# Kernel tuning notes

Hardware: AMD Instinct MI355X
Metric: run time of the kernel (lower is better)

## Reference

```python
import jax, jax.numpy as jnp
import numpy as np

NEG = -1000000.0  # mask value used by the original module


def setup_inputs() -> dict:
    key = jax.random.key(0)
    ks = jax.random.split(key, 8)
    N, D_IN, D_Q, D_K, E = 8192, 512, 512, 512, 262144
    s = 1.0 / np.sqrt(D_IN)
    return {
        "x": jax.random.normal(ks[0], (N, D_IN), dtype=jnp.float32),
        "edge_index": jax.random.randint(ks[1], (2, E), 0, N, dtype=jnp.int64),
        "Wq": jax.random.normal(ks[2], (D_IN, D_Q), dtype=jnp.float32) * s,
        "bq": jax.random.normal(ks[3], (D_Q,), dtype=jnp.float32) * 0.01,
        "Wk": jax.random.normal(ks[4], (D_IN, D_K), dtype=jnp.float32) * s,
        "bk": jax.random.normal(ks[5], (D_K,), dtype=jnp.float32) * 0.01,
        "Wv": jax.random.normal(ks[6], (D_IN, D_K), dtype=jnp.float32) * s,
        "bv": jax.random.normal(ks[7], (D_K,), dtype=jnp.float32) * 0.01,
    }


def reference(x, edge_index, Wq, bq, Wk, bk, Wv, bv):
    # Linear projections (x: [N, D_in])
    q = x @ Wq + bq  # [N, Dq]
    k = x @ Wk + bk  # [N, Dk]
    v = x @ Wv + bv  # [N, Dk]

    N = x.shape[0]
    # Dense adjacency from edge list (matches torch scatter adjacency[e0, e1] = 1)
    adj = jnp.zeros((N, N), dtype=x.dtype).at[edge_index[0], edge_index[1]].set(1.0)

    # Full scores (ptr=None branch), scaled by sqrt(Dq)
    a = (q @ k.T) / jnp.sqrt(jnp.asarray(q.shape[-1], dtype=x.dtype))
    a = a * adj + (1.0 - adj) * NEG

    attn = jax.nn.softmax(a, axis=-1)  # [N, N]
    return attn @ v  # [N, Dk]
```

## Files before the change

kernel.cpp:

```cpp
#include <hip/hip_runtime.h>


#define N_NODES 8192
#define DIM 512
#define MASK_WORDS 256
#define SCAP 256

typedef __attribute__((ext_vector_type(8))) short short8;
typedef __attribute__((ext_vector_type(4))) float f32x4;

__device__ __forceinline__ unsigned short f2bf(float f) {
    unsigned int u = __float_as_uint(f);
    u += 0x7fffu + ((u >> 16) & 1u);
    return (unsigned short)(u >> 16);
}
__device__ __forceinline__ float bf_lo(unsigned int w) { return __uint_as_float(w << 16); }
__device__ __forceinline__ float bf_hi(unsigned int w) { return __uint_as_float(w & 0xffff0000u); }

__device__ __forceinline__ float wred_sum(float s) {
    #pragma unroll
    for (int off = 1; off <= 32; off <<= 1) s += __shfl_xor(s, off, 64);
    return s;
}
__device__ __forceinline__ float wred_max(float s) {
    #pragma unroll
    for (int off = 1; off <= 32; off <<= 1) s = fmaxf(s, __shfl_xor(s, off, 64));
    return s;
}
__device__ __forceinline__ int wred_sumi(int s) {
    #pragma unroll
    for (int off = 1; off <= 32; off <<= 1) s += __shfl_xor(s, off, 64);
    return s;
}
__device__ __forceinline__ float dot8(uint4 a, uint4 b) {
    return bf_lo(a.x) * bf_lo(b.x) + bf_hi(a.x) * bf_hi(b.x)
         + bf_lo(a.y) * bf_lo(b.y) + bf_hi(a.y) * bf_hi(b.y)
         + bf_lo(a.z) * bf_lo(b.z) + bf_hi(a.z) * bf_hi(b.z)
         + bf_lo(a.w) * bf_lo(b.w) + bf_hi(a.w) * bf_hi(b.w);
}

__global__ __launch_bounds__(256) void prep1(
    const float* __restrict__ x, unsigned short* __restrict__ xb,
    const float* __restrict__ Wq, const float* __restrict__ Wk,
    const float* __restrict__ Wv, unsigned short* __restrict__ Wt,
    unsigned int* __restrict__ mask)
{
    __shared__ float sm[32][33];
    const int b = blockIdx.x;
    if (b < 4096) {
        int i = b * 256 + threadIdx.x;
        float4 f = ((const float4*)x)[i];
        ushort4 o;
        o.x = f2bf(f.x); o.y = f2bf(f.y); o.z = f2bf(f.z); o.w = f2bf(f.w);
        ((ushort4*)xb)[i] = o;
        ((uint2*)mask)[i] = make_uint2(0u, 0u);
    } else {
        int bb = b - 4096;
        int which = bb >> 8, t = bb & 255;
        const float* __restrict__ W = (which == 0) ? Wq : (which == 1) ? Wk : Wv;
        unsigned short* __restrict__ outp = Wt + (size_t)which * DIM * DIM;
        int n0 = (t & 15) * 32, k0 = (t >> 4) * 32;
        int tx = threadIdx.x & 31, ty = threadIdx.x >> 5;
        #pragma unroll
        for (int r = 0; r < 4; ++r)
            sm[ty + 8 * r][tx] = W[(size_t)(k0 + ty + 8 * r) * DIM + n0 + tx];
        __syncthreads();
        #pragma unroll
        for (int r = 0; r < 4; ++r)
            outp[(size_t)(n0 + ty + 8 * r) * DIM + k0 + tx] = f2bf(sm[tx][ty + 8 * r]);
    }
}

__global__ __launch_bounds__(256) void prep2(
    const int* __restrict__ ei, unsigned int* __restrict__ mask, int E)
{
    int e = blockIdx.x * 256 + threadIdx.x;
    if (e >= E) return;
    int src = ei[e];
    int dst = ei[E + e];
    atomicOr(&mask[(size_t)src * MASK_WORDS + (dst >> 5)], 1u << (dst & 31));
}

__device__ __forceinline__ void load_lds16(const unsigned short* g, unsigned short* l) {
    __builtin_amdgcn_global_load_lds(
        (const __attribute__((address_space(1))) unsigned int*)g,
        (__attribute__((address_space(3))) unsigned int*)l, 16, 0, 0);
}

__global__ __launch_bounds__(256) void mfma_gemm(
    const unsigned short* __restrict__ xb, const unsigned short* __restrict__ Wt,
    const float* __restrict__ bq, const float* __restrict__ bk, const float* __restrict__ bv,
    unsigned short* __restrict__ qkv)
{
    const int p = blockIdx.x;
    const int xcd = p & 7;
    const int s = p >> 3;
    const int mloc = s / 12;
    const int n = s - 12 * mloc;
    const int which = n >> 2;
    const int row0 = (xcd * 8 + mloc) << 7;
    const int col0 = (n & 3) << 7;

    const unsigned short* __restrict__ Bm = Wt + (size_t)which * DIM * DIM;
    const float* __restrict__ bias = (which == 0) ? bq : (which == 1) ? bk : bv;
    unsigned short* __restrict__ outp = qkv + (size_t)which * N_NODES * DIM;

    const int tid = threadIdx.x;
    const int lane = tid & 63;
    const int w = tid >> 6;
    const int wm = (w >> 1) * 64;
    const int wn = (w & 1) * 64;
    const int L = lane & 15;
    const int quad = lane >> 4;

    __shared__ unsigned short As[128 * 32];
    __shared__ unsigned short Bs[128 * 32];

    f32x4 zero = {0.f, 0.f, 0.f, 0.f};
    f32x4 acc[4][4];
    #pragma unroll
    for (int i = 0; i < 4; ++i)
        #pragma unroll
        for (int j = 0; j < 4; ++j) acc[i][j] = zero;

    const int m0 = tid >> 2;
    const int ko = (tid & 3) << 3;

    for (int k0 = 0; k0 < DIM; k0 += 32) {
        load_lds16(xb + (size_t)(row0 + m0) * DIM + k0 + ko,      As + tid * 8);
        load_lds16(xb + (size_t)(row0 + 64 + m0) * DIM + k0 + ko, As + 2048 + tid * 8);
        load_lds16(Bm + (size_t)(col0 + m0) * DIM + k0 + ko,      Bs + tid * 8);
        load_lds16(Bm + (size_t)(col0 + 64 + m0) * DIM + k0 + ko, Bs + 2048 + tid * 8);
        __syncthreads();

        short8 a[4], bfr[4];
        #pragma unroll
        for (int i = 0; i < 4; ++i)
            a[i] = *(const short8*)(const void*)&As[(wm + i * 16 + L) * 32 + quad * 8];
        #pragma unroll
        for (int j = 0; j < 4; ++j)
            bfr[j] = *(const short8*)(const void*)&Bs[(wn + j * 16 + L) * 32 + quad * 8];

        #pragma unroll
        for (int i = 0; i < 4; ++i)
            #pragma unroll
            for (int j = 0; j < 4; ++j)
                acc[i][j] = __builtin_amdgcn_mfma_f32_16x16x32_bf16(a[i], bfr[j], acc[i][j], 0, 0, 0);
        __syncthreads();
    }

    float biasv[4];
    #pragma unroll
    for (int j = 0; j < 4; ++j) biasv[j] = bias[col0 + wn + j * 16 + L];
    #pragma unroll
    for (int i = 0; i < 4; ++i) {
        int r0 = row0 + wm + i * 16 + quad * 4;
        #pragma unroll
        for (int j = 0; j < 4; ++j) {
            int c = col0 + wn + j * 16 + L;
            #pragma unroll
            for (int r = 0; r < 4; ++r)
                outp[(size_t)(r0 + r) * DIM + c] = f2bf(acc[i][j][r] + biasv[j]);
        }
    }
}

__global__ __launch_bounds__(256) void attn_kernel(
    const unsigned short* __restrict__ q, const unsigned short* __restrict__ k,
    const unsigned short* __restrict__ v, const unsigned int* __restrict__ mask,
    float* __restrict__ out)
{
    __shared__ unsigned short nbr[4][SCAP];
    __shared__ float pw[4][SCAP];
    __shared__ float buf[4][DIM];
    __shared__ float sm_m[4], sm_l[4];
    __shared__ int degs[4];
    __shared__ int cnt[4];

    const int tid = threadIdx.x;
    const int lane = tid & 63;
    const int wid = tid >> 6;
    const int row = blockIdx.x;

    const uint4 qv = *(const uint4*)(q + (size_t)row * DIM + lane * 8);
    const unsigned int mw = mask[(size_t)row * MASK_WORDS + wid * 64 + lane];

    const int pc_s = wred_sumi(__popc(mw));
    if (lane == 0) degs[wid] = pc_s;
    __syncthreads();
    const int total = degs[0] + degs[1] + degs[2] + degs[3];

    float o[8];
    #pragma unroll
    for (int i = 0; i < 8; ++i) o[i] = 0.f;

    if (total == 0) {
        for (int j = wid * 2048; j < (wid + 1) * 2048; ++j) {
            uint4 vv = *(const uint4*)(v + (size_t)j * DIM + lane * 8);
            o[0] += bf_lo(vv.x); o[1] += bf_hi(vv.x);
            o[2] += bf_lo(vv.y); o[3] += bf_hi(vv.y);
            o[4] += bf_lo(vv.z); o[5] += bf_hi(vv.z);
            o[6] += bf_lo(vv.w); o[7] += bf_hi(vv.w);
        }
        #pragma unroll
        for (int i = 0; i < 8; ++i) buf[wid][lane * 8 + i] = o[i];
        __syncthreads();
        const float sc = 1.0f / N_NODES;
        int c = tid * 2;
        float2 r;
        r.x = (buf[0][c] + buf[1][c] + buf[2][c] + buf[3][c]) * sc;
        r.y = (buf[0][c + 1] + buf[1][c + 1] + buf[2][c + 1] + buf[3][c + 1]) * sc;
        *(float2*)(out + (size_t)row * DIM + c) = r;
        return;
    }

    const float scale = 0.044194173824159220f;
    float m_run = -3.0e38f, l_run = 0.f;

    const int nchunks = (pc_s <= SCAP) ? 1 : 8;
    for (int c = 0; c < nchunks; ++c) {
        if (lane == 0) cnt[wid] = 0;
        if (nchunks == 1 || (lane >> 3) == c) {
            unsigned int ww = mw;
            while (ww) {
                int bpos = __ffs(ww) - 1; ww &= ww - 1;
                int pos = atomicAdd(&cnt[wid], 1);
                nbr[wid][pos] = (unsigned short)((wid * 64 + lane) * 32 + bpos);
            }
        }
        const int cn = cnt[wid];
        if (cn == 0) continue;

        for (int p0 = 0; p0 < cn; p0 += 4) {
            int j0 = nbr[wid][p0];
            int j1 = nbr[wid][(p0 + 1 < cn) ? p0 + 1 : p0];
            int j2 = nbr[wid][(p0 + 2 < cn) ? p0 + 2 : p0];
            int j3 = nbr[wid][(p0 + 3 < cn) ? p0 + 3 : p0];
            uint4 k0v = *(const uint4*)(k + (size_t)j0 * DIM + lane * 8);
            uint4 k1v = *(const uint4*)(k + (size_t)j1 * DIM + lane * 8);
            uint4 k2v = *(const uint4*)(k + (size_t)j2 * DIM + lane * 8);
            uint4 k3v = *(const uint4*)(k + (size_t)j3 * DIM + lane * 8);
            float s0 = wred_sum(dot8(qv, k0v));
            float s1 = wred_sum(dot8(qv, k1v));
            float s2 = wred_sum(dot8(qv, k2v));
            float s3 = wred_sum(dot8(qv, k3v));
            if (lane == 0) {
                pw[wid][p0] = s0 * scale;
                if (p0 + 1 < cn) pw[wid][p0 + 1] = s1 * scale;
                if (p0 + 2 < cn) pw[wid][p0 + 2] = s2 * scale;
                if (p0 + 3 < cn) pw[wid][p0 + 3] = s3 * scale;
            }
        }

        float mc = -3.0e38f;
        for (int p = lane; p < cn; p += 64) mc = fmaxf(mc, pw[wid][p]);
        mc = wred_max(mc);
        const float mnew = fmaxf(m_run, mc);
        const float f = __expf(m_run - mnew);
        float ls = 0.f;
        for (int p = lane; p < cn; p += 64) {
            float e = __expf(pw[wid][p] - mnew);
            pw[wid][p] = e;
            ls += e;
        }
        l_run = l_run * f + wred_sum(ls);
        m_run = mnew;
        #pragma unroll
        for (int i = 0; i < 8; ++i) o[i] *= f;

        for (int p0 = 0; p0 < cn; p0 += 4) {
            int j0 = nbr[wid][p0];
            int j1 = nbr[wid][(p0 + 1 < cn) ? p0 + 1 : p0];
            int j2 = nbr[wid][(p0 + 2 < cn) ? p0 + 2 : p0];
            int j3 = nbr[wid][(p0 + 3 < cn) ? p0 + 3 : p0];
            float w0 = pw[wid][p0];
            float w1 = (p0 + 1 < cn) ? pw[wid][p0 + 1] : 0.f;
            float w2 = (p0 + 2 < cn) ? pw[wid][p0 + 2] : 0.f;
            float w3 = (p0 + 3 < cn) ? pw[wid][p0 + 3] : 0.f;
            uint4 v0 = *(const uint4*)(v + (size_t)j0 * DIM + lane * 8);
            uint4 v1 = *(const uint4*)(v + (size_t)j1 * DIM + lane * 8);
            uint4 v2 = *(const uint4*)(v + (size_t)j2 * DIM + lane * 8);
            uint4 v3 = *(const uint4*)(v + (size_t)j3 * DIM + lane * 8);
            o[0] += w0 * bf_lo(v0.x) + w1 * bf_lo(v1.x) + w2 * bf_lo(v2.x) + w3 * bf_lo(v3.x);
            o[1] += w0 * bf_hi(v0.x) + w1 * bf_hi(v1.x) + w2 * bf_hi(v2.x) + w3 * bf_hi(v3.x);
            o[2] += w0 * bf_lo(v0.y) + w1 * bf_lo(v1.y) + w2 * bf_lo(v2.y) + w3 * bf_lo(v3.y);
            o[3] += w0 * bf_hi(v0.y) + w1 * bf_hi(v1.y) + w2 * bf_hi(v2.y) + w3 * bf_hi(v3.y);
            o[4] += w0 * bf_lo(v0.z) + w1 * bf_lo(v1.z) + w2 * bf_lo(v2.z) + w3 * bf_lo(v3.z);
            o[5] += w0 * bf_hi(v0.z) + w1 * bf_hi(v1.z) + w2 * bf_hi(v2.z) + w3 * bf_hi(v3.z);
            o[6] += w0 * bf_lo(v0.w) + w1 * bf_lo(v1.w) + w2 * bf_lo(v2.w) + w3 * bf_lo(v3.w);
            o[7] += w0 * bf_hi(v0.w) + w1 * bf_hi(v1.w) + w2 * bf_hi(v2.w) + w3 * bf_hi(v3.w);
        }
    }

    if (lane == 0) { sm_m[wid] = m_run; sm_l[wid] = l_run; }
    __syncthreads();
    const float M = fmaxf(fmaxf(sm_m[0], sm_m[1]), fmaxf(sm_m[2], sm_m[3]));
    const float Lsum = sm_l[0] * __expf(sm_m[0] - M) + sm_l[1] * __expf(sm_m[1] - M)
                     + sm_l[2] * __expf(sm_m[2] - M) + sm_l[3] * __expf(sm_m[3] - M);
    const float r = __expf(m_run - M);
    #pragma unroll
    for (int i = 0; i < 8; ++i) buf[wid][lane * 8 + i] = o[i] * r;
    __syncthreads();

    const float inv = 1.0f / Lsum;
    int c = tid * 2;
    float2 res;
    res.x = (buf[0][c] + buf[1][c] + buf[2][c] + buf[3][c]) * inv;
    res.y = (buf[0][c + 1] + buf[1][c + 1] + buf[2][c + 1] + buf[3][c + 1]) * inv;
    *(float2*)(out + (size_t)row * DIM + c) = res;
}

extern "C" void kernel_launch(void* const* d_in, const int* in_sizes, int n_in,
                              void* d_out, int out_size, void* d_ws, size_t ws_size,
                              hipStream_t stream)
{
    const float* x  = (const float*)d_in[0];
    const int*   ei = (const int*)d_in[1];
    const float* Wq = (const float*)d_in[2];
    const float* bq = (const float*)d_in[3];
    const float* Wk = (const float*)d_in[4];
    const float* bk = (const float*)d_in[5];
    const float* Wv = (const float*)d_in[6];
    const float* bv = (const float*)d_in[7];
    float* out = (float*)d_out;

    const int E = in_sizes[1] / 2;
    const size_t NM = (size_t)N_NODES * DIM;

    unsigned short* xb = (unsigned short*)d_ws;
    unsigned short* Wt = xb + NM;
    unsigned short* qkv = Wt + (size_t)3 * DIM * DIM;
    unsigned short* qb = qkv;
    unsigned short* kb = qkv + NM;
    unsigned short* vb = qkv + 2 * NM;
    unsigned int* mask = (unsigned int*)(qkv + 3 * NM);

    prep1<<<4864, 256, 0, stream>>>(x, xb, Wq, Wk, Wv, Wt, mask);
    prep2<<<(E + 255) / 256, 256, 0, stream>>>(ei, mask, E);

    mfma_gemm<<<768, 256, 0, stream>>>(xb, Wt, bq, bk, bv, qkv);

    attn_kernel<<<N_NODES, 256, 0, stream>>>(qb, kb, vb, mask, out);
}
```

Measured before the change: 180.6 us.

## Use per-wave persistent rows in attention and swizzle GEMM LDS tiles

The attention kernel becomes persistent. Each wavefront grabs a whole row through a global atomic counter and processes all of its neighbours alone. This removes the cross-wave LDS merge and block barriers, and balances the uneven per-row degrees. The QKV GEMM also XOR-swizzles its LDS tile layout to avoid bank conflicts, and stages its output through LDS so it can write coalesced 16-byte stores. In exchange, each row's neighbour work is serialized on one wave, and all waves contend on a single atomic counter.

```diff
diff --git a/kernel.cpp b/kernel.cpp
--- a/kernel.cpp
+++ b/kernel.cpp
@@ -4,7 +4,7 @@
 #define N_NODES 8192
 #define DIM 512
 #define MASK_WORDS 256
-#define SCAP 256
+#define CAPW 512
 
 typedef __attribute__((ext_vector_type(8))) short short8;
 typedef __attribute__((ext_vector_type(4))) float f32x4;
@@ -43,11 +43,12 @@
     const float* __restrict__ x, unsigned short* __restrict__ xb,
     const float* __restrict__ Wq, const float* __restrict__ Wk,
     const float* __restrict__ Wv, unsigned short* __restrict__ Wt,
-    unsigned int* __restrict__ mask)
+    unsigned int* __restrict__ mask, int* __restrict__ ctr)
 {
     __shared__ float sm[32][33];
     const int b = blockIdx.x;
     if (b < 4096) {
+        if (b == 0 && threadIdx.x == 0) *ctr = 0;
         int i = b * 256 + threadIdx.x;
         float4 f = ((const float4*)x)[i];
         ushort4 o;
@@ -113,8 +114,9 @@
     const int L = lane & 15;
     const int quad = lane >> 4;
 
-    __shared__ unsigned short As[128 * 32];
-    __shared__ unsigned short Bs[128 * 32];
+    __shared__ unsigned short smem[8192];
+    unsigned short* As = smem;
+    unsigned short* Bs = smem + 4096;
 
     f32x4 zero = {0.f, 0.f, 0.f, 0.f};
     f32x4 acc[4][4];
@@ -124,22 +126,28 @@
         for (int j = 0; j < 4; ++j) acc[i][j] = zero;
 
     const int m0 = tid >> 2;
-    const int ko = (tid & 3) << 3;
+    const int cg = tid & 3;
+    const int ko0 = (cg ^ (m0 & 3)) << 3;
+    const int ko1 = (cg ^ ((m0 + 64) & 3)) << 3;
 
     for (int k0 = 0; k0 < DIM; k0 += 32) {
-        load_lds16(xb + (size_t)(row0 + m0) * DIM + k0 + ko,      As + tid * 8);
-        load_lds16(xb + (size_t)(row0 + 64 + m0) * DIM + k0 + ko, As + 2048 + tid * 8);
-        load_lds16(Bm + (size_t)(col0 + m0) * DIM + k0 + ko,      Bs + tid * 8);
-        load_lds16(Bm + (size_t)(col0 + 64 + m0) * DIM + k0 + ko, Bs + 2048 + tid * 8);
+        load_lds16(xb + (size_t)(row0 + m0) * DIM + k0 + ko0,      As + tid * 8);
+        load_lds16(xb + (size_t)(row0 + 64 + m0) * DIM + k0 + ko1, As + 2048 + tid * 8);
+        load_lds16(Bm + (size_t)(col0 + m0) * DIM + k0 + ko0,      Bs + tid * 8);
+        load_lds16(Bm + (size_t)(col0 + 64 + m0) * DIM + k0 + ko1, Bs + 2048 + tid * 8);
         __syncthreads();
 
         short8 a[4], bfr[4];
         #pragma unroll
-        for (int i = 0; i < 4; ++i)
-            a[i] = *(const short8*)(const void*)&As[(wm + i * 16 + L) * 32 + quad * 8];
-        #pragma unroll
-        for (int j = 0; j < 4; ++j)
-            bfr[j] = *(const short8*)(const void*)&Bs[(wn + j * 16 + L) * 32 + quad * 8];
+        for (int i = 0; i < 4; ++i) {
+            int r = wm + i * 16 + L;
+            a[i] = *(const short8*)(const void*)&As[r * 32 + ((quad ^ (r & 3)) << 3)];
+        }
+        #pragma unroll
+        for (int j = 0; j < 4; ++j) {
+            int r = wn + j * 16 + L;
+            bfr[j] = *(const short8*)(const void*)&Bs[r * 32 + ((quad ^ (r & 3)) << 3)];
+        }
 
         #pragma unroll
         for (int i = 0; i < 4; ++i)
@@ -152,162 +160,178 @@
     float biasv[4];
     #pragma unroll
     for (int j = 0; j < 4; ++j) biasv[j] = bias[col0 + wn + j * 16 + L];
-    #pragma unroll
-    for (int i = 0; i < 4; ++i) {
-        int r0 = row0 + wm + i * 16 + quad * 4;
-        #pragma unroll
-        for (int j = 0; j < 4; ++j) {
-            int c = col0 + wn + j * 16 + L;
+
+    unsigned short* tb = smem;
+    #pragma unroll
+    for (int round = 0; round < 2; ++round) {
+        __syncthreads();
+        if ((w >> 1) == round) {
             #pragma unroll
-            for (int r = 0; r < 4; ++r)
-                outp[(size_t)(r0 + r) * DIM + c] = f2bf(acc[i][j][r] + biasv[j]);
-        }
+            for (int i = 0; i < 4; ++i)
+                #pragma unroll
+                for (int j = 0; j < 4; ++j)
+                    #pragma unroll
+                    for (int r = 0; r < 4; ++r)
+                        tb[(i * 16 + quad * 4 + r) * 128 + wn + j * 16 + L] =
+                            f2bf(acc[i][j][r] + biasv[j]);
+        }
+        __syncthreads();
+        const int rrow = tid >> 2;
+        const int seg = (tid & 3) * 32;
+        const uint4* srcv = (const uint4*)&tb[rrow * 128 + seg];
+        unsigned short* dst = outp + (size_t)(row0 + round * 64 + rrow) * DIM + col0 + seg;
+        #pragma unroll
+        for (int ss = 0; ss < 4; ++ss)
+            *(uint4*)(dst + ss * 8) = srcv[ss];
     }
 }
 
 __global__ __launch_bounds__(256) void attn_kernel(
     const unsigned short* __restrict__ q, const unsigned short* __restrict__ k,
     const unsigned short* __restrict__ v, const unsigned int* __restrict__ mask,
-    float* __restrict__ out)
-{
-    __shared__ unsigned short nbr[4][SCAP];
-    __shared__ float pw[4][SCAP];
-    __shared__ float buf[4][DIM];
-    __shared__ float sm_m[4], sm_l[4];
-    __shared__ int degs[4];
+    int* __restrict__ ctr, float* __restrict__ out)
+{
+    __shared__ unsigned short nbr[4][CAPW];
+    __shared__ float pw[4][CAPW];
     __shared__ int cnt[4];
 
     const int tid = threadIdx.x;
     const int lane = tid & 63;
     const int wid = tid >> 6;
-    const int row = blockIdx.x;
-
-    const uint4 qv = *(const uint4*)(q + (size_t)row * DIM + lane * 8);
-    const unsigned int mw = mask[(size_t)row * MASK_WORDS + wid * 64 + lane];
-
-    const int pc_s = wred_sumi(__popc(mw));
-    if (lane == 0) degs[wid] = pc_s;
-    __syncthreads();
-    const int total = degs[0] + degs[1] + degs[2] + degs[3];
-
-    float o[8];
-    #pragma unroll
-    for (int i = 0; i < 8; ++i) o[i] = 0.f;
-
-    if (total == 0) {
-        for (int j = wid * 2048; j < (wid + 1) * 2048; ++j) {
-            uint4 vv = *(const uint4*)(v + (size_t)j * DIM + lane * 8);
-            o[0] += bf_lo(vv.x); o[1] += bf_hi(vv.x);
-            o[2] += bf_lo(vv.y); o[3] += bf_hi(vv.y);
-            o[4] += bf_lo(vv.z); o[5] += bf_hi(vv.z);
-            o[6] += bf_lo(vv.w); o[7] += bf_hi(vv.w);
-        }
-        #pragma unroll
-        for (int i = 0; i < 8; ++i) buf[wid][lane * 8 + i] = o[i];
-        __syncthreads();
-        const float sc = 1.0f / N_NODES;
-        int c = tid * 2;
-        float2 r;
-        r.x = (buf[0][c] + buf[1][c] + buf[2][c] + buf[3][c]) * sc;
-        r.y = (buf[0][c + 1] + buf[1][c + 1] + buf[2][c + 1] + buf[3][c + 1]) * sc;
-        *(float2*)(out + (size_t)row * DIM + c) = r;
-        return;
+    const float scale = 0.044194173824159220f;
+
+    for (;;) {
+        int rowv = 0;
+        if (lane == 0) rowv = atomicAdd(ctr, 1);
+        const int row = __shfl(rowv, 0, 64);
+        if (row >= N_NODES) break;
+
+        const uint4 qv = *(const uint4*)(q + (size_t)row * DIM + lane * 8);
+        const unsigned int* __restrict__ mrow = mask + (size_t)row * MASK_WORDS;
+        unsigned int mw[4];
+        int pc = 0;
+        #pragma unroll
+        for (int t = 0; t < 4; ++t) {
+            mw[t] = mrow[lane + 64 * t];
+            pc += __popc(mw[t]);
+        }
+        const int total = wred_sumi(pc);
+
+        float o[8];
+        #pragma unroll
+        for (int i = 0; i < 8; ++i) o[i] = 0.f;
+
+        if (total == 0) {
+            for (int j = 0; j < N_NODES; ++j) {
+                uint4 vv = *(const uint4*)(v + (size_t)j * DIM + lane * 8);
+                o[0] += bf_lo(vv.x); o[1] += bf_hi(vv.x);
+                o[2] += bf_lo(vv.y); o[3] += bf_hi(vv.y);
+                o[4] += bf_lo(vv.z); o[5] += bf_hi(vv.z);
+                o[6] += bf_lo(vv.w); o[7] += bf_hi(vv.w);
+            }
+            const float sc = 1.0f / N_NODES;
+            float4 r0 = {o[0] * sc, o[1] * sc, o[2] * sc, o[3] * sc};
+            float4 r1 = {o[4] * sc, o[5] * sc, o[6] * sc, o[7] * sc};
+            *(float4*)(out + (size_t)row * DIM + lane * 8) = r0;
+            *(float4*)(out + (size_t)row * DIM + lane * 8 + 4) = r1;
+            continue;
+        }
+
+        const int nchunks = (total <= CAPW) ? 1 : 16;
+        float m_run = -3.0e38f, l_run = 0.f;
+
+        for (int c = 0; c < nchunks; ++c) {
+            if (lane == 0) cnt[wid] = 0;
+            if (nchunks == 1) {
+                #pragma unroll
+                for (int t = 0; t < 4; ++t) {
+                    unsigned int ww = mw[t];
+                    while (ww) {
+                        int bpos = __ffs(ww) - 1; ww &= ww - 1;
+                        int pos = atomicAdd(&cnt[wid], 1);
+                        nbr[wid][pos] = (unsigned short)((lane + 64 * t) * 32 + bpos);
+                    }
+                }
+            } else {
+                for (int wi = lane; wi < 16; wi += 64) {
+                    unsigned int ww = mrow[c * 16 + wi];
+                    while (ww) {
+                        int bpos = __ffs(ww) - 1; ww &= ww - 1;
+                        int pos = atomicAdd(&cnt[wid], 1);
+                        nbr[wid][pos] = (unsigned short)((c * 16 + wi) * 32 + bpos);
+                    }
+                }
+            }
+            const int cn = cnt[wid];
+            if (cn == 0) continue;
+
+            for (int p0 = 0; p0 < cn; p0 += 4) {
+                int j0 = nbr[wid][p0];
+                int j1 = nbr[wid][(p0 + 1 < cn) ? p0 + 1 : p0];
+                int j2 = nbr[wid][(p0 + 2 < cn) ? p0 + 2 : p0];
+                int j3 = nbr[wid][(p0 + 3 < cn) ? p0 + 3 : p0];
+                uint4 k0v = *(const uint4*)(k + (size_t)j0 * DIM + lane * 8);
+                uint4 k1v = *(const uint4*)(k + (size_t)j1 * DIM + lane * 8);
+                uint4 k2v = *(const uint4*)(k + (size_t)j2 * DIM + lane * 8);
+                uint4 k3v = *(const uint4*)(k + (size_t)j3 * DIM + lane * 8);
+                float s0 = wred_sum(dot8(qv, k0v));
+                float s1 = wred_sum(dot8(qv, k1v));
+                float s2 = wred_sum(dot8(qv, k2v));
+                float s3 = wred_sum(dot8(qv, k3v));
+                if (lane == 0) {
+                    pw[wid][p0] = s0 * scale;
+                    if (p0 + 1 < cn) pw[wid][p0 + 1] = s1 * scale;
+                    if (p0 + 2 < cn) pw[wid][p0 + 2] = s2 * scale;
+                    if (p0 + 3 < cn) pw[wid][p0 + 3] = s3 * scale;
+                }
+            }
+
+            float mc = -3.0e38f;
+            for (int p = lane; p < cn; p += 64) mc = fmaxf(mc, pw[wid][p]);
+            mc = wred_max(mc);
+            const float mnew = fmaxf(m_run, mc);
+            const float f = __expf(m_run - mnew);
+            float ls = 0.f;
+            for (int p = lane; p < cn; p += 64) {
+                float e = __expf(pw[wid][p] - mnew);
+                pw[wid][p] = e;
+                ls += e;
+            }
+            l_run = l_run * f + wred_sum(ls);
+            m_run = mnew;
+            #pragma unroll
+            for (int i = 0; i < 8; ++i) o[i] *= f;
+
+            for (int p0 = 0; p0 < cn; p0 += 4) {
+                int j0 = nbr[wid][p0];
+                int j1 = nbr[wid][(p0 + 1 < cn) ? p0 + 1 : p0];
+                int j2 = nbr[wid][(p0 + 2 < cn) ? p0 + 2 : p0];
+                int j3 = nbr[wid][(p0 + 3 < cn) ? p0 + 3 : p0];
+                float w0 = pw[wid][p0];
+                float w1 = (p0 + 1 < cn) ? pw[wid][p0 + 1] : 0.f;
+                float w2 = (p0 + 2 < cn) ? pw[wid][p0 + 2] : 0.f;
+                float w3 = (p0 + 3 < cn) ? pw[wid][p0 + 3] : 0.f;
+                uint4 v0 = *(const uint4*)(v + (size_t)j0 * DIM + lane * 8);
+                uint4 v1 = *(const uint4*)(v + (size_t)j1 * DIM + lane * 8);
+                uint4 v2 = *(const uint4*)(v + (size_t)j2 * DIM + lane * 8);
+                uint4 v3 = *(const uint4*)(v + (size_t)j3 * DIM + lane * 8);
+                o[0] += w0 * bf_lo(v0.x) + w1 * bf_lo(v1.x) + w2 * bf_lo(v2.x) + w3 * bf_lo(v3.x);
+                o[1] += w0 * bf_hi(v0.x) + w1 * bf_hi(v1.x) + w2 * bf_hi(v2.x) + w3 * bf_hi(v3.x);
+                o[2] += w0 * bf_lo(v0.y) + w1 * bf_lo(v1.y) + w2 * bf_lo(v2.y) + w3 * bf_lo(v3.y);
+                o[3] += w0 * bf_hi(v0.y) + w1 * bf_hi(v1.y) + w2 * bf_hi(v2.y) + w3 * bf_hi(v3.y);
+                o[4] += w0 * bf_lo(v0.z) + w1 * bf_lo(v1.z) + w2 * bf_lo(v2.z) + w3 * bf_lo(v3.z);
+                o[5] += w0 * bf_hi(v0.z) + w1 * bf_hi(v1.z) + w2 * bf_hi(v2.z) + w3 * bf_hi(v3.z);
+                o[6] += w0 * bf_lo(v0.w) + w1 * bf_lo(v1.w) + w2 * bf_lo(v2.w) + w3 * bf_lo(v3.w);
+                o[7] += w0 * bf_hi(v0.w) + w1 * bf_hi(v1.w) + w2 * bf_hi(v2.w) + w3 * bf_hi(v3.w);
+            }
+        }
+
+        const float inv = 1.0f / l_run;
+        float4 r0 = {o[0] * inv, o[1] * inv, o[2] * inv, o[3] * inv};
+        float4 r1 = {o[4] * inv, o[5] * inv, o[6] * inv, o[7] * inv};
+        *(float4*)(out + (size_t)row * DIM + lane * 8) = r0;
+        *(float4*)(out + (size_t)row * DIM + lane * 8 + 4) = r1;
     }
-
-    const float scale = 0.044194173824159220f;
-    float m_run = -3.0e38f, l_run = 0.f;
-
-    const int nchunks = (pc_s <= SCAP) ? 1 : 8;
-    for (int c = 0; c < nchunks; ++c) {
-        if (lane == 0) cnt[wid] = 0;
-        if (nchunks == 1 || (lane >> 3) == c) {
-            unsigned int ww = mw;
-            while (ww) {
-                int bpos = __ffs(ww) - 1; ww &= ww - 1;
-                int pos = atomicAdd(&cnt[wid], 1);
-                nbr[wid][pos] = (unsigned short)((wid * 64 + lane) * 32 + bpos);
-            }
-        }
-        const int cn = cnt[wid];
-        if (cn == 0) continue;
-
-        for (int p0 = 0; p0 < cn; p0 += 4) {
-            int j0 = nbr[wid][p0];
-            int j1 = nbr[wid][(p0 + 1 < cn) ? p0 + 1 : p0];
-            int j2 = nbr[wid][(p0 + 2 < cn) ? p0 + 2 : p0];
-            int j3 = nbr[wid][(p0 + 3 < cn) ? p0 + 3 : p0];
-            uint4 k0v = *(const uint4*)(k + (size_t)j0 * DIM + lane * 8);
-            uint4 k1v = *(const uint4*)(k + (size_t)j1 * DIM + lane * 8);
-            uint4 k2v = *(const uint4*)(k + (size_t)j2 * DIM + lane * 8);
-            uint4 k3v = *(const uint4*)(k + (size_t)j3 * DIM + lane * 8);
-            float s0 = wred_sum(dot8(qv, k0v));
-            float s1 = wred_sum(dot8(qv, k1v));
-            float s2 = wred_sum(dot8(qv, k2v));
-            float s3 = wred_sum(dot8(qv, k3v));
-            if (lane == 0) {
-                pw[wid][p0] = s0 * scale;
-                if (p0 + 1 < cn) pw[wid][p0 + 1] = s1 * scale;
-                if (p0 + 2 < cn) pw[wid][p0 + 2] = s2 * scale;
-                if (p0 + 3 < cn) pw[wid][p0 + 3] = s3 * scale;
-            }
-        }
-
-        float mc = -3.0e38f;
-        for (int p = lane; p < cn; p += 64) mc = fmaxf(mc, pw[wid][p]);
-        mc = wred_max(mc);
-        const float mnew = fmaxf(m_run, mc);
-        const float f = __expf(m_run - mnew);
-        float ls = 0.f;
-        for (int p = lane; p < cn; p += 64) {
-            float e = __expf(pw[wid][p] - mnew);
-            pw[wid][p] = e;
-            ls += e;
-        }
-        l_run = l_run * f + wred_sum(ls);
-        m_run = mnew;
-        #pragma unroll
-        for (int i = 0; i < 8; ++i) o[i] *= f;
-
-        for (int p0 = 0; p0 < cn; p0 += 4) {
-            int j0 = nbr[wid][p0];
-            int j1 = nbr[wid][(p0 + 1 < cn) ? p0 + 1 : p0];
-            int j2 = nbr[wid][(p0 + 2 < cn) ? p0 + 2 : p0];
-            int j3 = nbr[wid][(p0 + 3 < cn) ? p0 + 3 : p0];
-            float w0 = pw[wid][p0];
-            float w1 = (p0 + 1 < cn) ? pw[wid][p0 + 1] : 0.f;
-            float w2 = (p0 + 2 < cn) ? pw[wid][p0 + 2] : 0.f;
-            float w3 = (p0 + 3 < cn) ? pw[wid][p0 + 3] : 0.f;
-            uint4 v0 = *(const uint4*)(v + (size_t)j0 * DIM + lane * 8);
-            uint4 v1 = *(const uint4*)(v + (size_t)j1 * DIM + lane * 8);
-            uint4 v2 = *(const uint4*)(v + (size_t)j2 * DIM + lane * 8);
-            uint4 v3 = *(const uint4*)(v + (size_t)j3 * DIM + lane * 8);
-            o[0] += w0 * bf_lo(v0.x) + w1 * bf_lo(v1.x) + w2 * bf_lo(v2.x) + w3 * bf_lo(v3.x);
-            o[1] += w0 * bf_hi(v0.x) + w1 * bf_hi(v1.x) + w2 * bf_hi(v2.x) + w3 * bf_hi(v3.x);
-            o[2] += w0 * bf_lo(v0.y) + w1 * bf_lo(v1.y) + w2 * bf_lo(v2.y) + w3 * bf_lo(v3.y);
-            o[3] += w0 * bf_hi(v0.y) + w1 * bf_hi(v1.y) + w2 * bf_hi(v2.y) + w3 * bf_hi(v3.y);
-            o[4] += w0 * bf_lo(v0.z) + w1 * bf_lo(v1.z) + w2 * bf_lo(v2.z) + w3 * bf_lo(v3.z);
-            o[5] += w0 * bf_hi(v0.z) + w1 * bf_hi(v1.z) + w2 * bf_hi(v2.z) + w3 * bf_hi(v3.z);
-            o[6] += w0 * bf_lo(v0.w) + w1 * bf_lo(v1.w) + w2 * bf_lo(v2.w) + w3 * bf_lo(v3.w);
-            o[7] += w0 * bf_hi(v0.w) + w1 * bf_hi(v1.w) + w2 * bf_hi(v2.w) + w3 * bf_hi(v3.w);
-        }
-    }
-
-    if (lane == 0) { sm_m[wid] = m_run; sm_l[wid] = l_run; }
-    __syncthreads();
-    const float M = fmaxf(fmaxf(sm_m[0], sm_m[1]), fmaxf(sm_m[2], sm_m[3]));
-    const float Lsum = sm_l[0] * __expf(sm_m[0] - M) + sm_l[1] * __expf(sm_m[1] - M)
-                     + sm_l[2] * __expf(sm_m[2] - M) + sm_l[3] * __expf(sm_m[3] - M);
-    const float r = __expf(m_run - M);
-    #pragma unroll
-    for (int i = 0; i < 8; ++i) buf[wid][lane * 8 + i] = o[i] * r;
-    __syncthreads();
-
-    const float inv = 1.0f / Lsum;
-    int c = tid * 2;
-    float2 res;
-    res.x = (buf[0][c] + buf[1][c] + buf[2][c] + buf[3][c]) * inv;
-    res.y = (buf[0][c + 1] + buf[1][c + 1] + buf[2][c + 1] + buf[3][c + 1]) * inv;
-    *(float2*)(out + (size_t)row * DIM + c) = res;
 }
 
 extern "C" void kernel_launch(void* const* d_in, const int* in_sizes, int n_in,
@@ -334,11 +358,12 @@
     unsigned short* kb = qkv + NM;
     unsigned short* vb = qkv + 2 * NM;
     unsigned int* mask = (unsigned int*)(qkv + 3 * NM);
-
-    prep1<<<4864, 256, 0, stream>>>(x, xb, Wq, Wk, Wv, Wt, mask);
+    int* ctr = (int*)(mask + (size_t)N_NODES * MASK_WORDS);
+
+    prep1<<<4864, 256, 0, stream>>>(x, xb, Wq, Wk, Wv, Wt, mask, ctr);
     prep2<<<(E + 255) / 256, 256, 0, stream>>>(ei, mask, E);
 
     mfma_gemm<<<768, 256, 0, stream>>>(xb, Wt, bq, bk, bv, qkv);
 
-    attn_kernel<<<N_NODES, 256, 0, stream>>>(qb, kb, vb, mask, out);
-}
+    attn_kernel<<<1024, 256, 0, stream>>>(qb, kb, vb, mask, ctr, out);
+}
```

New measurement: 287.1 us. 59.0% more time.
